# Kernel optimization log

Measured on AMD Instinct MI355X. Metric: run time of the kernel, lower is better.

The kernel has to match this reference:

```python
import jax, jax.numpy as jnp
import numpy as np

# Model constants (from init parameters)
H = 2048            # prediction_horizon
B = 8192            # batch of parallel rollouts
WHEELBASE = 2.5
MAX_STEER = 0.5
DT = 0.05
MAX_ACC = 5000.0 / 1000.0  # engine_force / mass


def setup_inputs() -> dict:
    key = jax.random.key(0)
    k0, k1, k2, k3, k4, k5 = jax.random.split(key, 6)
    return {
        "start_x": jax.random.normal(k0, (B,), dtype=jnp.float32),
        "start_y": jax.random.normal(k1, (B,), dtype=jnp.float32),
        "start_yaw": jax.random.normal(k2, (B,), dtype=jnp.float32),
        "start_speed": jax.random.uniform(k3, (B,), dtype=jnp.float32) * 10.0,
        "accel": jax.random.normal(k4, (H,), dtype=jnp.float32),     # per-step throttle params
        "steering": jax.random.normal(k5, (H,), dtype=jnp.float32),  # per-step steering params
    }


def reference(start_x, start_y, start_yaw, start_speed, accel, steering):
    """Kinematic bicycle-model rollout over the prediction horizon.

    Returns (x, y, yaw, speed), each [H, B], with step 0 = the start state,
    matching the torch module's state lists.
    """

    def step(carry, ctrl):
        x, y, yaw, speed = carry
        a, s = ctrl
        throttle = jnp.clip(a, -1.0, 1.0)
        new_speed = speed + DT * throttle * MAX_ACC
        steer = jnp.clip(s, -MAX_STEER, MAX_STEER)
        ang_vel = speed * jnp.tan(steer) / WHEELBASE
        new_x = x + speed * jnp.cos(yaw) * DT
        new_y = y + speed * jnp.sin(yaw) * DT
        new_yaw = yaw + ang_vel * DT
        new = (new_x, new_y, new_yaw, new_speed)
        return new, new

    init = (start_x, start_y, start_yaw, start_speed)
    # Steps i = 0..H-2 use controls[i]; controls[H-1] is unused, as in the torch loop.
    _, (xs, ys, yaws, speeds) = jax.lax.scan(step, init, (accel[:-1], steering[:-1]))

    x_all = jnp.concatenate([start_x[None], xs], axis=0)        # [H, B]
    y_all = jnp.concatenate([start_y[None], ys], axis=0)
    yaw_all = jnp.concatenate([start_yaw[None], yaws], axis=0)
    speed_all = jnp.concatenate([start_speed[None], speeds], axis=0)
    return (x_all, y_all, yaw_all, speed_all)
```

## Files before the change

### kernel.cpp

```cpp
#include <hip/hip_runtime.h>
#include <math.h>

#define H   2048
#define NB  8192
#define KCH 64
#define LCH 32
#define BPC 8

#define DT_F 0.05f

static_assert(KCH * LCH == H, "chunking must cover H");
static_assert(BPC * 1024 == NB, "b-tiling must cover NB");

typedef float f32x4 __attribute__((ext_vector_type(4)));

__global__ __launch_bounds__(1024) void precomp_scan(
    const float* __restrict__ accel, const float* __restrict__ steering,
    float* __restrict__ Cv, float* __restrict__ Av, float* __restrict__ Bv) {
  __shared__ double l1[1024];
  __shared__ double l2[1024];
  const int t = threadIdx.x;

  double dv[2], w[2], Cl[2];
  for (int m = 0; m < 2; ++m) {
    int j = t * 2 + m;
    if (j < H - 1) {
      float a = accel[j];    a = fminf(1.0f, fmaxf(-1.0f, a));
      float s = steering[j]; s = fminf(0.5f, fmaxf(-0.5f, s));
      dv[m] = 0.25 * (double)a;
      w[m]  = 0.02 * tan((double)s);
    } else {
      dv[m] = 0.0; w[m] = 0.0;
    }
  }

  {
    double tot1 = dv[0] + dv[1];
    double tot2 = w[0] + w[1];
    double run1 = tot1, run2 = tot2;
    l1[t] = run1; l2[t] = run2; __syncthreads();
    for (int off = 1; off < 1024; off <<= 1) {
      double y1 = (t >= off) ? l1[t - off] : 0.0;
      double y2 = (t >= off) ? l2[t - off] : 0.0;
      __syncthreads();
      run1 += y1; run2 += y2;
      l1[t] = run1; l2[t] = run2; __syncthreads();
    }
    double e1 = run1 - tot1;
    double e2 = run2 - tot2;
    Cl[0] = e1; Cv[t * 2] = (float)e1; Av[t * 2] = (float)e2;
    e1 += dv[0]; e2 += w[0];
    Cl[1] = e1; Cv[t * 2 + 1] = (float)e1; Av[t * 2 + 1] = (float)e2;
  }
  __syncthreads();

  {
    double v0 = Cl[0] * w[0];
    double v1 = Cl[1] * w[1];
    double tot = v0 + v1;
    double run = tot;
    l1[t] = run; __syncthreads();
    for (int off = 1; off < 1024; off <<= 1) {
      double y = (t >= off) ? l1[t - off] : 0.0;
      __syncthreads();
      run += y; l1[t] = run; __syncthreads();
    }
    double e = run - tot;
    Bv[t * 2] = (float)e; e += v0;
    Bv[t * 2 + 1] = (float)e;
  }
}

__global__ __launch_bounds__(256) void yaw_speed_partials(
    const float* __restrict__ syaw, const float* __restrict__ sspd,
    const float* __restrict__ Cv, const float* __restrict__ Av,
    const float* __restrict__ Bv,
    float* __restrict__ out, float* __restrict__ px, float* __restrict__ py) {
  __shared__ float sC[LCH], sA[LCH], sB[LCH];
  const int k  = blockIdx.x >> 3;
  const int b  = ((blockIdx.x & (BPC - 1)) << 10) + (threadIdx.x << 2);
  const int j0 = k * LCH;
  if (threadIdx.x < LCH) {
    sC[threadIdx.x] = Cv[j0 + threadIdx.x];
    sA[threadIdx.x] = Av[j0 + threadIdx.x];
    sB[threadIdx.x] = Bv[j0 + threadIdx.x];
  }
  __syncthreads();

  const f32x4 yaw0v = *(const f32x4*)(syaw + b);
  const f32x4 s0v   = *(const f32x4*)(sspd + b);
  float yaw0[4] = {yaw0v.x, yaw0v.y, yaw0v.z, yaw0v.w};
  float s0[4]   = {s0v.x, s0v.y, s0v.z, s0v.w};
  float accx[4] = {0.f, 0.f, 0.f, 0.f};
  float accy[4] = {0.f, 0.f, 0.f, 0.f};
  float* __restrict__ oy = out + 2 * (size_t)H * NB;
  float* __restrict__ os = out + 3 * (size_t)H * NB;

  for (int m = 0; m < LCH; ++m) {
    const float C  = sC[m];
    const float A  = sA[m];
    const float Bc = sB[m];
    float spd[4], yw[4], sn[4], cs[4];
#pragma unroll
    for (int q = 0; q < 4; ++q) {
      spd[q] = s0[q] + C;
      yw[q]  = fmaf(s0[q], A, yaw0[q]) + Bc;
      __sincosf(yw[q], &sn[q], &cs[q]);
    }
    const size_t idx = (size_t)(j0 + m) * NB + b;
    f32x4 ywv, spdv;
    ywv.x = yw[0]; ywv.y = yw[1]; ywv.z = yw[2]; ywv.w = yw[3];
    spdv.x = spd[0]; spdv.y = spd[1]; spdv.z = spd[2]; spdv.w = spd[3];
    __builtin_nontemporal_store(ywv,  (f32x4*)(oy + idx));
    __builtin_nontemporal_store(spdv, (f32x4*)(os + idx));
#pragma unroll
    for (int q = 0; q < 4; ++q) {
      accx[q] = fmaf(spd[q], cs[q], accx[q]);
      accy[q] = fmaf(spd[q], sn[q], accy[q]);
    }
  }
  f32x4 axv, ayv;
  axv.x = accx[0]; axv.y = accx[1]; axv.z = accx[2]; axv.w = accx[3];
  ayv.x = accy[0]; ayv.y = accy[1]; ayv.z = accy[2]; ayv.w = accy[3];
  *(f32x4*)(px + (size_t)k * NB + b) = axv;
  *(f32x4*)(py + (size_t)k * NB + b) = ayv;
}

__global__ __launch_bounds__(256) void chunk_scan(
    const float* __restrict__ px, const float* __restrict__ py,
    float* __restrict__ ox, float* __restrict__ oyv) {
  const int b = blockIdx.x * 256 + threadIdx.x;
  float ax = 0.0f, ay = 0.0f;
  for (int k = 0; k < KCH; ++k) {
    float tx = px[(size_t)k * NB + b];
    float ty = py[(size_t)k * NB + b];
    ox[(size_t)k * NB + b]  = ax;
    oyv[(size_t)k * NB + b] = ay;
    ax += tx;
    ay += ty;
  }
}

__global__ __launch_bounds__(256) void xy_write(
    const float* __restrict__ sx, const float* __restrict__ sy,
    const float* __restrict__ syaw, const float* __restrict__ sspd,
    const float* __restrict__ Cv, const float* __restrict__ Av,
    const float* __restrict__ Bv,
    const float* __restrict__ ox, const float* __restrict__ oyv,
    float* __restrict__ out) {
  __shared__ float sC[LCH], sA[LCH], sB[LCH];
  const int k  = blockIdx.x >> 3;
  const int b  = ((blockIdx.x & (BPC - 1)) << 10) + (threadIdx.x << 2);
  const int j0 = k * LCH;
  if (threadIdx.x < LCH) {
    sC[threadIdx.x] = Cv[j0 + threadIdx.x];
    sA[threadIdx.x] = Av[j0 + threadIdx.x];
    sB[threadIdx.x] = Bv[j0 + threadIdx.x];
  }
  __syncthreads();

  const f32x4 x0v   = *(const f32x4*)(sx + b);
  const f32x4 y0v   = *(const f32x4*)(sy + b);
  const f32x4 yaw0v = *(const f32x4*)(syaw + b);
  const f32x4 s0v   = *(const f32x4*)(sspd + b);
  const f32x4 rxv   = *(const f32x4*)(ox  + (size_t)k * NB + b);
  const f32x4 ryv   = *(const f32x4*)(oyv + (size_t)k * NB + b);
  float x0[4]   = {x0v.x, x0v.y, x0v.z, x0v.w};
  float y0[4]   = {y0v.x, y0v.y, y0v.z, y0v.w};
  float yaw0[4] = {yaw0v.x, yaw0v.y, yaw0v.z, yaw0v.w};
  float s0[4]   = {s0v.x, s0v.y, s0v.z, s0v.w};
  float rx[4]   = {rxv.x, rxv.y, rxv.z, rxv.w};
  float ry[4]   = {ryv.x, ryv.y, ryv.z, ryv.w};
  float* __restrict__ outx = out;
  float* __restrict__ outy = out + (size_t)H * NB;

  for (int m = 0; m < LCH; ++m) {
    const float C  = sC[m];
    const float A  = sA[m];
    const float Bc = sB[m];
    float spd[4], yw[4], sn[4], cs[4], wx[4], wy[4];
#pragma unroll
    for (int q = 0; q < 4; ++q) {
      spd[q] = s0[q] + C;
      yw[q]  = fmaf(s0[q], A, yaw0[q]) + Bc;
      __sincosf(yw[q], &sn[q], &cs[q]);
      wx[q] = fmaf(DT_F, rx[q], x0[q]);
      wy[q] = fmaf(DT_F, ry[q], y0[q]);
    }
    const size_t idx = (size_t)(j0 + m) * NB + b;
    f32x4 wxv, wyv;
    wxv.x = wx[0]; wxv.y = wx[1]; wxv.z = wx[2]; wxv.w = wx[3];
    wyv.x = wy[0]; wyv.y = wy[1]; wyv.z = wy[2]; wyv.w = wy[3];
    __builtin_nontemporal_store(wxv, (f32x4*)(outx + idx));
    __builtin_nontemporal_store(wyv, (f32x4*)(outy + idx));
#pragma unroll
    for (int q = 0; q < 4; ++q) {
      rx[q] = fmaf(spd[q], cs[q], rx[q]);
      ry[q] = fmaf(spd[q], sn[q], ry[q]);
    }
  }
}

extern "C" void kernel_launch(void* const* d_in, const int* in_sizes, int n_in,
                              void* d_out, int out_size, void* d_ws, size_t ws_size,
                              hipStream_t stream) {
  const float* start_x     = (const float*)d_in[0];
  const float* start_y     = (const float*)d_in[1];
  const float* start_yaw   = (const float*)d_in[2];
  const float* start_speed = (const float*)d_in[3];
  const float* accel       = (const float*)d_in[4];
  const float* steering    = (const float*)d_in[5];
  float* out = (float*)d_out;

  float* ws = (float*)d_ws;
  float* Cv  = ws;
  float* Av  = ws + H;
  float* Bv  = ws + 2 * H;
  float* px  = ws + 3 * H;
  float* py  = px + (size_t)KCH * NB;
  float* ox  = py + (size_t)KCH * NB;
  float* oyv = ox + (size_t)KCH * NB;

  precomp_scan<<<1, 1024, 0, stream>>>(accel, steering, Cv, Av, Bv);
  yaw_speed_partials<<<KCH * BPC, 256, 0, stream>>>(start_yaw, start_speed,
                                                    Cv, Av, Bv, out, px, py);
  chunk_scan<<<NB / 256, 256, 0, stream>>>(px, py, ox, oyv);
  xy_write<<<KCH * BPC, 256, 0, stream>>>(start_x, start_y, start_yaw, start_speed,
                                          Cv, Av, Bv, ox, oyv, out);
}
```

Before: 289.7 us.

## Use wave-shuffle scans in precompute and parallelize chunk scan with interleaved xy buffers

The single-block precompute scan replaces its shared-memory Hillis-Steele loops, which used many block barriers, with wavefront shuffle scans plus a small cross-wave pass. The chunk scan, which used only 32 blocks each walking 64 chunks serially, now splits the chunk axis across four waves per block. It combines their partial sums through shared memory and launches 128 blocks. The x/y partials are stored interleaved as float2 so each kernel needs one vector access stream instead of two. The risks are extra register pressure from the 16-element arrays and a changed float summation order in the chunk scan.

```diff
diff --git a/kernel.cpp b/kernel.cpp
--- a/kernel.cpp
+++ b/kernel.cpp
@@ -17,11 +17,13 @@
 __global__ __launch_bounds__(1024) void precomp_scan(
     const float* __restrict__ accel, const float* __restrict__ steering,
     float* __restrict__ Cv, float* __restrict__ Av, float* __restrict__ Bv) {
-  __shared__ double l1[1024];
-  __shared__ double l2[1024];
-  const int t = threadIdx.x;
-
-  double dv[2], w[2], Cl[2];
+  __shared__ double wsum1[16], wsum2[16];
+  __shared__ double woff1[16], woff2[16];
+  const int t    = threadIdx.x;
+  const int lane = t & 63;
+  const int wid  = t >> 6;
+
+  double dv[2], w[2];
   for (int m = 0; m < 2; ++m) {
     int j = t * 2 + m;
     if (j < H - 1) {
@@ -34,48 +36,65 @@
     }
   }
 
-  {
-    double tot1 = dv[0] + dv[1];
-    double tot2 = w[0] + w[1];
-    double run1 = tot1, run2 = tot2;
-    l1[t] = run1; l2[t] = run2; __syncthreads();
-    for (int off = 1; off < 1024; off <<= 1) {
-      double y1 = (t >= off) ? l1[t - off] : 0.0;
-      double y2 = (t >= off) ? l2[t - off] : 0.0;
-      __syncthreads();
-      run1 += y1; run2 += y2;
-      l1[t] = run1; l2[t] = run2; __syncthreads();
-    }
-    double e1 = run1 - tot1;
-    double e2 = run2 - tot2;
-    Cl[0] = e1; Cv[t * 2] = (float)e1; Av[t * 2] = (float)e2;
-    e1 += dv[0]; e2 += w[0];
-    Cl[1] = e1; Cv[t * 2 + 1] = (float)e1; Av[t * 2 + 1] = (float)e2;
-  }
-  __syncthreads();
-
-  {
-    double v0 = Cl[0] * w[0];
-    double v1 = Cl[1] * w[1];
-    double tot = v0 + v1;
-    double run = tot;
-    l1[t] = run; __syncthreads();
-    for (int off = 1; off < 1024; off <<= 1) {
-      double y = (t >= off) ? l1[t - off] : 0.0;
-      __syncthreads();
-      run += y; l1[t] = run; __syncthreads();
-    }
-    double e = run - tot;
-    Bv[t * 2] = (float)e; e += v0;
-    Bv[t * 2 + 1] = (float)e;
-  }
+  double p1 = dv[0] + dv[1];
+  double p2 = w[0] + w[1];
+  double i1 = p1, i2 = p2;
+  for (int off = 1; off < 64; off <<= 1) {
+    double u1 = __shfl_up(i1, (unsigned)off);
+    double u2 = __shfl_up(i2, (unsigned)off);
+    if (lane >= off) { i1 += u1; i2 += u2; }
+  }
+  if (lane == 63) { wsum1[wid] = i1; wsum2[wid] = i2; }
+  __syncthreads();
+  if (wid == 0) {
+    double v1 = (lane < 16) ? wsum1[lane] : 0.0;
+    double v2 = (lane < 16) ? wsum2[lane] : 0.0;
+    double s1 = v1, s2 = v2;
+    for (int off = 1; off < 16; off <<= 1) {
+      double u1 = __shfl_up(s1, (unsigned)off);
+      double u2 = __shfl_up(s2, (unsigned)off);
+      if (lane >= off) { s1 += u1; s2 += u2; }
+    }
+    if (lane < 16) { woff1[lane] = s1 - v1; woff2[lane] = s2 - v2; }
+  }
+  __syncthreads();
+  double e1 = woff1[wid] + (i1 - p1);
+  double e2 = woff2[wid] + (i2 - p2);
+  double C0 = e1,          A0 = e2;
+  double C1 = e1 + dv[0],  A1 = e2 + w[0];
+  Cv[t * 2]     = (float)C0;  Av[t * 2]     = (float)A0;
+  Cv[t * 2 + 1] = (float)C1;  Av[t * 2 + 1] = (float)A1;
+
+  double v0 = C0 * w[0];
+  double v1 = C1 * w[1];
+  double p3 = v0 + v1;
+  double i3 = p3;
+  for (int off = 1; off < 64; off <<= 1) {
+    double u3 = __shfl_up(i3, (unsigned)off);
+    if (lane >= off) i3 += u3;
+  }
+  if (lane == 63) wsum1[wid] = i3;
+  __syncthreads();
+  if (wid == 0) {
+    double v3 = (lane < 16) ? wsum1[lane] : 0.0;
+    double s3 = v3;
+    for (int off = 1; off < 16; off <<= 1) {
+      double u3 = __shfl_up(s3, (unsigned)off);
+      if (lane >= off) s3 += u3;
+    }
+    if (lane < 16) woff1[lane] = s3 - v3;
+  }
+  __syncthreads();
+  double e3 = woff1[wid] + (i3 - p3);
+  Bv[t * 2]     = (float)e3;
+  Bv[t * 2 + 1] = (float)(e3 + v0);
 }
 
 __global__ __launch_bounds__(256) void yaw_speed_partials(
     const float* __restrict__ syaw, const float* __restrict__ sspd,
     const float* __restrict__ Cv, const float* __restrict__ Av,
     const float* __restrict__ Bv,
-    float* __restrict__ out, float* __restrict__ px, float* __restrict__ py) {
+    float* __restrict__ out, float2* __restrict__ pxy) {
   __shared__ float sC[LCH], sA[LCH], sB[LCH];
   const int k  = blockIdx.x >> 3;
   const int b  = ((blockIdx.x & (BPC - 1)) << 10) + (threadIdx.x << 2);
@@ -119,25 +138,43 @@
       accy[q] = fmaf(spd[q], sn[q], accy[q]);
     }
   }
-  f32x4 axv, ayv;
-  axv.x = accx[0]; axv.y = accx[1]; axv.z = accx[2]; axv.w = accx[3];
-  ayv.x = accy[0]; ayv.y = accy[1]; ayv.z = accy[2]; ayv.w = accy[3];
-  *(f32x4*)(px + (size_t)k * NB + b) = axv;
-  *(f32x4*)(py + (size_t)k * NB + b) = ayv;
+  f32x4 p01, p23;
+  p01.x = accx[0]; p01.y = accy[0]; p01.z = accx[1]; p01.w = accy[1];
+  p23.x = accx[2]; p23.y = accy[2]; p23.z = accx[3]; p23.w = accy[3];
+  f32x4* pp = (f32x4*)(pxy + (size_t)k * NB + b);
+  pp[0] = p01;
+  pp[1] = p23;
 }
 
 __global__ __launch_bounds__(256) void chunk_scan(
-    const float* __restrict__ px, const float* __restrict__ py,
-    float* __restrict__ ox, float* __restrict__ oyv) {
-  const int b = blockIdx.x * 256 + threadIdx.x;
-  float ax = 0.0f, ay = 0.0f;
-  for (int k = 0; k < KCH; ++k) {
-    float tx = px[(size_t)k * NB + b];
-    float ty = py[(size_t)k * NB + b];
-    ox[(size_t)k * NB + b]  = ax;
-    oyv[(size_t)k * NB + b] = ay;
-    ax += tx;
-    ay += ty;
+    const float2* __restrict__ pxy, float2* __restrict__ oxy) {
+  __shared__ float sx_[4][64];
+  __shared__ float sy_[4][64];
+  const int q = threadIdx.x >> 6;
+  const int i = threadIdx.x & 63;
+  const int b = blockIdx.x * 64 + i;
+
+  float vx[16], vy[16];
+  float ax = 0.f, ay = 0.f;
+#pragma unroll
+  for (int kk = 0; kk < 16; ++kk) {
+    const int k = q * 16 + kk;
+    float2 v = pxy[(size_t)k * NB + b];
+    vx[kk] = v.x; vy[kk] = v.y;
+    ax += v.x; ay += v.y;
+  }
+  sx_[q][i] = ax; sy_[q][i] = ay;
+  __syncthreads();
+
+  float ox = 0.f, oy = 0.f;
+  for (int qq = 0; qq < q; ++qq) { ox += sx_[qq][i]; oy += sy_[qq][i]; }
+
+#pragma unroll
+  for (int kk = 0; kk < 16; ++kk) {
+    const int k = q * 16 + kk;
+    float2 o; o.x = ox; o.y = oy;
+    oxy[(size_t)k * NB + b] = o;
+    ox += vx[kk]; oy += vy[kk];
   }
 }
 
@@ -146,7 +183,7 @@
     const float* __restrict__ syaw, const float* __restrict__ sspd,
     const float* __restrict__ Cv, const float* __restrict__ Av,
     const float* __restrict__ Bv,
-    const float* __restrict__ ox, const float* __restrict__ oyv,
+    const float2* __restrict__ oxy,
     float* __restrict__ out) {
   __shared__ float sC[LCH], sA[LCH], sB[LCH];
   const int k  = blockIdx.x >> 3;
@@ -163,14 +200,15 @@
   const f32x4 y0v   = *(const f32x4*)(sy + b);
   const f32x4 yaw0v = *(const f32x4*)(syaw + b);
   const f32x4 s0v   = *(const f32x4*)(sspd + b);
-  const f32x4 rxv   = *(const f32x4*)(ox  + (size_t)k * NB + b);
-  const f32x4 ryv   = *(const f32x4*)(oyv + (size_t)k * NB + b);
+  const f32x4* op   = (const f32x4*)(oxy + (size_t)k * NB + b);
+  const f32x4 o01 = op[0];
+  const f32x4 o23 = op[1];
   float x0[4]   = {x0v.x, x0v.y, x0v.z, x0v.w};
   float y0[4]   = {y0v.x, y0v.y, y0v.z, y0v.w};
   float yaw0[4] = {yaw0v.x, yaw0v.y, yaw0v.z, yaw0v.w};
   float s0[4]   = {s0v.x, s0v.y, s0v.z, s0v.w};
-  float rx[4]   = {rxv.x, rxv.y, rxv.z, rxv.w};
-  float ry[4]   = {ryv.x, ryv.y, ryv.z, ryv.w};
+  float rx[4]   = {o01.x, o01.z, o23.x, o23.z};
+  float ry[4]   = {o01.y, o01.w, o23.y, o23.w};
   float* __restrict__ outx = out;
   float* __restrict__ outy = out + (size_t)H * NB;
 
@@ -216,15 +254,13 @@
   float* Cv  = ws;
   float* Av  = ws + H;
   float* Bv  = ws + 2 * H;
-  float* px  = ws + 3 * H;
-  float* py  = px + (size_t)KCH * NB;
-  float* ox  = py + (size_t)KCH * NB;
-  float* oyv = ox + (size_t)KCH * NB;
+  float2* pxy = (float2*)(ws + 4 * H);
+  float2* oxy = pxy + (size_t)KCH * NB;
 
   precomp_scan<<<1, 1024, 0, stream>>>(accel, steering, Cv, Av, Bv);
   yaw_speed_partials<<<KCH * BPC, 256, 0, stream>>>(start_yaw, start_speed,
-                                                    Cv, Av, Bv, out, px, py);
-  chunk_scan<<<NB / 256, 256, 0, stream>>>(px, py, ox, oyv);
+                                                    Cv, Av, Bv, out, pxy);
+  chunk_scan<<<NB / 64, 256, 0, stream>>>(pxy, oxy);
   xy_write<<<KCH * BPC, 256, 0, stream>>>(start_x, start_y, start_yaw, start_speed,
-                                          Cv, Av, Bv, ox, oyv, out);
-}
+                                          Cv, Av, Bv, oxy, out);
+}
```

After: 286.1 us. Within noise of the previous version (-1.3%).
